# Optimization experiments

Hardware: AMD Instinct MI355X
Metric: run time of the kernel (lower is better)

Reference implementation:

```python
import jax, jax.numpy as jnp
import numpy as np

HIDDEN = 1024
HEADS = 16
HEAD_DIM = HIDDEN // HEADS

def setup_inputs() -> dict:
    key = jax.random.key(0)
    k1, k2, k3 = jax.random.split(key, 3)
    scale = 1.0 / np.sqrt(HIDDEN)
    return {
        "x": jax.random.normal(k1, (2, 2048, HIDDEN), dtype=jnp.float32),
        "w_qkv": jax.random.normal(k2, (HIDDEN, 3 * HIDDEN), dtype=jnp.float32) * scale,
        "b_qkv": jnp.zeros((3 * HIDDEN,), dtype=jnp.float32),
        "w_out": jax.random.normal(k3, (HIDDEN, HIDDEN), dtype=jnp.float32) * scale,
        "b_out": jnp.zeros((HIDDEN,), dtype=jnp.float32),
    }

def reference(x, w_qkv, b_qkv, w_out, b_out):
    B, S, H = x.shape
    qkv = x @ w_qkv + b_qkv                              # (B,S,3H)
    qkv = qkv.reshape(B, S, 3, HEADS, HEAD_DIM)
    qkv = jnp.transpose(qkv, (2, 0, 3, 1, 4))            # (3,B,nh,S,hd)
    q, k, v = qkv[0], qkv[1], qkv[2]
    scores = jnp.einsum("bhqd,bhkd->bhqk", q, k) / np.sqrt(HEAD_DIM)
    causal = jnp.triu(jnp.ones((S, S), dtype=bool), k=1)  # True above diagonal
    scores = jnp.where(causal, -jnp.inf, scores)
    attn = jax.nn.softmax(scores, axis=-1)               # dropout: eval mode (identity)
    out = jnp.einsum("bhqk,bhkd->bhqd", attn, v)
    out = jnp.transpose(out, (0, 2, 1, 3)).reshape(B, S, H)
    return out @ w_out + b_out
```

## Files before the change

### kernel.cpp

```cpp
#include <hip/hip_runtime.h>
#include <hip/hip_bf16.h>

typedef short short8 __attribute__((ext_vector_type(8)));
typedef float f32x4 __attribute__((ext_vector_type(4)));

typedef const __attribute__((address_space(1))) unsigned int* gas_ptr;
typedef __attribute__((address_space(3))) unsigned int* las_ptr;
#define ASYNC16(g, l) __builtin_amdgcn_global_load_lds((gas_ptr)(g), (las_ptr)(l), 16, 0, 0)

__device__ __forceinline__ unsigned short f2bf(float f) {
    unsigned int u = __builtin_bit_cast(unsigned int, f);
    u += 0x7fff + ((u >> 16) & 1);
    return (unsigned short)(u >> 16);
}
__device__ __forceinline__ float bf2f(unsigned short s) {
    unsigned int u = (unsigned int)s << 16;
    return __builtin_bit_cast(float, u);
}
__device__ __forceinline__ unsigned int pkbf_trunc(float lo, float hi) {
    return __builtin_amdgcn_perm(__builtin_bit_cast(unsigned int, hi),
                                 __builtin_bit_cast(unsigned int, lo), 0x07060302u);
}

__device__ __forceinline__ void transpose_tile(
    const float* __restrict__ w, unsigned short* __restrict__ wt,
    int K, int N, int k0, int n0, unsigned short* tile)
{
    for (int i = threadIdx.x; i < 64 * 64; i += 256) {
        int r = i >> 6, c = i & 63;
        tile[r * 65 + c] = f2bf(w[(size_t)(k0 + r) * N + n0 + c]);
    }
    __syncthreads();
    for (int i = threadIdx.x; i < 64 * 64; i += 256) {
        int r = i >> 6, c = i & 63;
        wt[(size_t)(n0 + r) * K + k0 + c] = tile[c * 65 + r];
    }
}

__global__ __launch_bounds__(256) void prep(
    const float* __restrict__ x, const float* __restrict__ w_qkv,
    const float* __restrict__ w_out,
    unsigned short* __restrict__ x_b, unsigned short* __restrict__ wqkv_t,
    unsigned short* __restrict__ wout_t)
{
    __shared__ unsigned short tile[64 * 65];
    int bid = blockIdx.x;
    if (bid < 4096) {
        int i = (bid * 256 + threadIdx.x) * 4;
        float4 v = *(const float4*)(x + i);
        ushort4 o;
        o.x = f2bf(v.x); o.y = f2bf(v.y); o.z = f2bf(v.z); o.w = f2bf(v.w);
        *(ushort4*)(x_b + i) = o;
    } else if (bid < 4096 + 768) {
        int t = bid - 4096;
        transpose_tile(w_qkv, wqkv_t, 1024, 3072, (t / 48) * 64, (t % 48) * 64, tile);
    } else {
        int t = bid - 4864;
        transpose_tile(w_out, wout_t, 1024, 1024, (t >> 4) * 64, (t & 15) * 64, tile);
    }
}


template<bool OUT_BF16, bool QKV>
__global__ __launch_bounds__(256, 3) void gemm_bt(
    const unsigned short* __restrict__ A,
    const unsigned short* __restrict__ Bt,
    const float* __restrict__ bias,
    void* __restrict__ C,
    unsigned short* __restrict__ vTp,
    int M, int N, int K)
{
    __shared__ __align__(16) unsigned short As[128 * 32];
    __shared__ __align__(16) unsigned short Bs[128 * 32];
    const int tid = threadIdx.x;
    const int lane = tid & 63;
    const int wave = tid >> 6;
    const int wr = wave >> 1, wc = wave & 1;
    const int m0 = blockIdx.x * 128, n0 = blockIdx.y * 128;
    const int fr = lane & 15, fq = lane >> 4;

    f32x4 acc[4][4] = {};

    const int grow = lane >> 2;
    const int gcol = (lane & 3) * 8;
    const unsigned short* Ag = A  + (size_t)(m0 + wave * 32 + grow) * K + gcol;
    const unsigned short* Bg = Bt + (size_t)(n0 + wave * 32 + grow) * K + gcol;
    unsigned short* AsW0 = As + (wave * 32) * 32;
    unsigned short* AsW1 = As + (wave * 32 + 16) * 32;
    unsigned short* BsW0 = Bs + (wave * 32) * 32;
    unsigned short* BsW1 = Bs + (wave * 32 + 16) * 32;

    for (int k0 = 0; k0 < K; k0 += 32) {
        __syncthreads();
        ASYNC16(Ag + k0,          AsW0);
        ASYNC16(Ag + 16 * K + k0, AsW1);
        ASYNC16(Bg + k0,          BsW0);
        ASYNC16(Bg + 16 * K + k0, BsW1);
        __syncthreads();

        short8 af[4], bfr[4];
#pragma unroll
        for (int i = 0; i < 4; i++)
            af[i] = *(const short8*)(As + (wr * 64 + i * 16 + fr) * 32 + fq * 8);
#pragma unroll
        for (int j = 0; j < 4; j++)
            bfr[j] = *(const short8*)(Bs + (wc * 64 + j * 16 + fr) * 32 + fq * 8);
#pragma unroll
        for (int i = 0; i < 4; i++)
#pragma unroll
            for (int j = 0; j < 4; j++)
                acc[i][j] = __builtin_amdgcn_mfma_f32_16x16x32_bf16(af[i], bfr[j], acc[i][j], 0, 0, 0);
    }

#pragma unroll
    for (int i = 0; i < 4; i++)
#pragma unroll
        for (int j = 0; j < 4; j++) {
            int col = n0 + wc * 64 + j * 16 + fr;
            float bv = bias[col];
            if (QKV && col >= 2048) {
                int hh = (col - 2048) >> 6, d = col & 63;
#pragma unroll
                for (int r = 0; r < 4; r++) {
                    int row = m0 + wr * 64 + i * 16 + fq * 4 + r;
                    int bb = row >> 11, s = row & 2047;
                    vTp[((size_t)(bb * 16 + hh) * 64 + d) * 2048 + s] = f2bf(acc[i][j][r] + bv);
                }
            } else {
                const int cstride = QKV ? 2048 : N;
#pragma unroll
                for (int r = 0; r < 4; r++) {
                    int row = m0 + wr * 64 + i * 16 + fq * 4 + r;
                    float v = acc[i][j][r] + bv;
                    if (OUT_BF16)
                        ((unsigned short*)C)[(size_t)row * cstride + col] = f2bf(v);
                    else
                        ((float*)C)[(size_t)row * cstride + col] = v;
                }
            }
        }
}


template<int RG0>
__device__ __forceinline__ void attn_step(
    const unsigned short* __restrict__ Ks0, const unsigned short* __restrict__ Ks1,
    const unsigned short* __restrict__ Vs0, const unsigned short* __restrict__ Vs1,
    unsigned short* __restrict__ Psw,
    const short8 (&qf)[4][2], const short8 ones,
    f32x4 (&o_acc)[4][4], f32x4 (&l_acc)[4],
    int j0, int fr, int fq,
    const int (&qrow0)[4], bool diagA, bool diagB)
{
    short8 kf[4][2];
#pragma unroll
    for (int t = 0; t < 4; t++) {
        kf[t][0] = *(const short8*)(Ks0 + (t * 16 + fr) * 32 + fq * 8);
        kf[t][1] = *(const short8*)(Ks1 + (t * 16 + fr) * 32 + fq * 8);
    }

#pragma unroll
    for (int rg = RG0; rg < 4; rg++) {
        f32x4 s[4];
#pragma unroll
        for (int t = 0; t < 4; t++) {
            s[t] = (f32x4){0.f, 0.f, 0.f, 0.f};
            s[t] = __builtin_amdgcn_mfma_f32_16x16x32_bf16(qf[rg][0], kf[t][0], s[t], 0, 0, 0);
            s[t] = __builtin_amdgcn_mfma_f32_16x16x32_bf16(qf[rg][1], kf[t][1], s[t], 0, 0, 0);
        }
        const bool diag = (rg < 2) ? diagA : diagB;
        unsigned short* prow = Psw + rg * (16 * 64);
        if (diag) {
#pragma unroll
            for (int t = 0; t < 4; t++) {
                float p[4];
#pragma unroll
                for (int r = 0; r < 4; r++) {
                    float v = __expf(s[t][r] * 0.125f - 8.0f);
                    if ((j0 + t * 16 + fr) > (qrow0[rg] + fq * 4 + r)) v = 0.f;
                    p[r] = v;
                }
                unsigned int pk01 = pkbf_trunc(p[0], p[1]);
                unsigned int pk23 = pkbf_trunc(p[2], p[3]);
                int base = (fq * 4) * 64 + ((t * 16 + fr + 16 * fq) & 63);
                prow[base]       = (unsigned short)pk01;
                prow[base + 64]  = (unsigned short)(pk01 >> 16);
                prow[base + 128] = (unsigned short)pk23;
                prow[base + 192] = (unsigned short)(pk23 >> 16);
            }
        } else {
#pragma unroll
            for (int t = 0; t < 4; t++) {
                float p[4];
#pragma unroll
                for (int r = 0; r < 4; r++)
                    p[r] = __expf(s[t][r] * 0.125f - 8.0f);
                unsigned int pk01 = pkbf_trunc(p[0], p[1]);
                unsigned int pk23 = pkbf_trunc(p[2], p[3]);
                int base = (fq * 4) * 64 + ((t * 16 + fr + 16 * fq) & 63);
                prow[base]       = (unsigned short)pk01;
                prow[base + 64]  = (unsigned short)(pk01 >> 16);
                prow[base + 128] = (unsigned short)pk23;
                prow[base + 192] = (unsigned short)(pk23 >> 16);
            }
        }
    }

#pragma unroll
    for (int ks = 0; ks < 2; ks++) {
        const unsigned short* Vsb = ks ? Vs1 : Vs0;
        const int colp = (ks * 32 + fq * 8 + 16 * ((fr >> 2) & 3)) & 63;
        short8 pf[4];
#pragma unroll
        for (int rg = RG0; rg < 4; rg++)
            pf[rg] = *(const short8*)(Psw + rg * (16 * 64) + fr * 64 + colp);
#pragma unroll
        for (int t = 0; t < 4; t++) {
            short8 vf = *(const short8*)(Vsb + (t * 16 + fr) * 32 + fq * 8);
#pragma unroll
            for (int rg = RG0; rg < 4; rg++)
                o_acc[rg][t] = __builtin_amdgcn_mfma_f32_16x16x32_bf16(pf[rg], vf, o_acc[rg][t], 0, 0, 0);
        }
#pragma unroll
        for (int rg = RG0; rg < 4; rg++)
            l_acc[rg] = __builtin_amdgcn_mfma_f32_16x16x32_bf16(pf[rg], ones, l_acc[rg], 0, 0, 0);
    }
}

__global__ __launch_bounds__(128, 2) void flash_attn(
    const unsigned short* __restrict__ qkv,
    const unsigned short* __restrict__ vT,
    unsigned short* __restrict__ Opart,
    float* __restrict__ lpart)
{
    const int gid = blockIdx.x;
    const int bh = gid & 31;
    const int sl = gid >> 5;
    const int p  = sl & 15;
    const int g  = sl >> 4;
    const int h = bh & 15, b = bh >> 4;
    const int tid = threadIdx.x, wave = tid >> 6, lane = tid & 63;
    const int fr = lane & 15, fq = lane >> 4;
    const size_t RS = 2048;

    const unsigned short* Qb = qkv + (size_t)b * 2048 * RS + h * 64;
    const unsigned short* Kb = Qb + 1024;
    const unsigned short* Vt = vT + (size_t)(b * 16 + h) * 64 * 2048;

    __shared__ __align__(16) unsigned short Ks[2][64 * 32];
    __shared__ __align__(16) unsigned short Vs[2][64 * 32];
    __shared__ __align__(16) unsigned short Ps[2][4 * 16 * 64];

    short8 qf[4][2];
    int qrow0[4];
#pragma unroll
    for (int rg = 0; rg < 4; rg++) {
        int qt = (rg < 2) ? p : (31 - p);
        qrow0[rg] = qt * 64 + wave * 32 + (rg & 1) * 16;
        const unsigned short* qrow = Qb + (size_t)(qrow0[rg] + fr) * RS;
        qf[rg][0] = *(const short8*)(qrow + fq * 8);
        qf[rg][1] = *(const short8*)(qrow + 32 + fq * 8);
    }
    short8 ones;
#pragma unroll
    for (int e = 0; e < 8; e++) ones[e] = (short)0x3F80;

    f32x4 o_acc[4][4] = {};
    f32x4 l_acc[4] = {};

    const int grow = lane >> 2;
    const int gcol = (lane & 3) * 8;
    const unsigned short* Kg = Kb + (size_t)(wave * 32 + grow) * RS + gcol;
    const unsigned short* Vg = Vt + (size_t)(wave * 32 + grow) * 2048 + gcol;
    unsigned short* KsW00 = Ks[0] + (wave * 32) * 32;
    unsigned short* KsW01 = Ks[0] + (wave * 32 + 16) * 32;
    unsigned short* KsW10 = Ks[1] + (wave * 32) * 32;
    unsigned short* KsW11 = Ks[1] + (wave * 32 + 16) * 32;
    unsigned short* VsW00 = Vs[0] + (wave * 32) * 32;
    unsigned short* VsW01 = Vs[0] + (wave * 32 + 16) * 32;
    unsigned short* VsW10 = Vs[1] + (wave * 32) * 32;
    unsigned short* VsW11 = Vs[1] + (wave * 32 + 16) * 32;

    const int njt = 32 - p;
    int lo = (g == 0) ? 0 : njt;
    int hi = njt;
    {
        int cum = 0;
        bool flo = (g == 0), fhi = false;
        for (int j = 0; j < njt; j++) {
            if (!flo && cum >= 44 * g)        { lo = j; flo = true; }
            if (!fhi && cum >= 44 * (g + 1))  { hi = j; fhi = true; }
            cum += (j <= p) ? 8 : 4;
        }
    }

    for (int jt = lo; jt < hi; jt++) {
        const int j0 = jt * 64;
        __syncthreads();
        ASYNC16(Kg + (size_t)j0 * RS,               KsW00);
        ASYNC16(Kg + (size_t)(j0 + 16) * RS,        KsW01);
        ASYNC16(Kg + (size_t)j0 * RS + 32,          KsW10);
        ASYNC16(Kg + (size_t)(j0 + 16) * RS + 32,   KsW11);
        ASYNC16(Vg + j0,               VsW00);
        ASYNC16(Vg + 16 * 2048 + j0,   VsW01);
        ASYNC16(Vg + j0 + 32,          VsW10);
        ASYNC16(Vg + 16 * 2048 + j0 + 32, VsW11);
        __syncthreads();

        bool diagA = (jt == p), diagB = (jt == 31 - p);
        if (jt <= p)
            attn_step<0>(Ks[0], Ks[1], Vs[0], Vs[1], Ps[wave], qf, ones,
                         o_acc, l_acc, j0, fr, fq, qrow0, diagA, diagB);
        else
            attn_step<2>(Ks[0], Ks[1], Vs[0], Vs[1], Ps[wave], qf, ones,
                         o_acc, l_acc, j0, fr, fq, qrow0, diagA, diagB);
    }

    unsigned short* Og = Opart + (size_t)g * 4096 * 1024;
    float* lg = lpart + (size_t)g * 4096 * 16;
#pragma unroll
    for (int rg = 0; rg < 4; rg++) {
#pragma unroll
        for (int t = 0; t < 4; t++)
#pragma unroll
            for (int r = 0; r < 4; r++) {
                int row = qrow0[rg] + fq * 4 + r;
                Og[(size_t)(b * 2048 + row) * 1024 + h * 64 + t * 16 + fr] = f2bf(o_acc[rg][t][r]);
            }
        if (fr == 0) {
#pragma unroll
            for (int r = 0; r < 4; r++) {
                int row = qrow0[rg] + fq * 4 + r;
                lg[(size_t)(b * 2048 + row) * 16 + h] = l_acc[rg][r];
            }
        }
    }
}

__global__ __launch_bounds__(256) void reduce_attn(
    const unsigned short* __restrict__ Opart, const float* __restrict__ lpart,
    unsigned short* __restrict__ out)
{
    const size_t OP = (size_t)4096 * 1024, LP = (size_t)4096 * 16;
    int i = (blockIdx.x * 256 + threadIdx.x) * 8;
    int row = i >> 10, h = (i & 1023) >> 6;
    float lsum = lpart[row * 16 + h] + lpart[LP + row * 16 + h] + lpart[2 * LP + row * 16 + h];
    float inv = 1.0f / lsum;
    float acc[8];
#pragma unroll
    for (int e = 0; e < 8; e++) acc[e] = 0.f;
#pragma unroll
    for (int gpart = 0; gpart < 3; gpart++) {
        ushort4 a0 = *(const ushort4*)(Opart + gpart * OP + i);
        ushort4 a1 = *(const ushort4*)(Opart + gpart * OP + i + 4);
        acc[0] += bf2f(a0.x); acc[1] += bf2f(a0.y); acc[2] += bf2f(a0.z); acc[3] += bf2f(a0.w);
        acc[4] += bf2f(a1.x); acc[5] += bf2f(a1.y); acc[6] += bf2f(a1.z); acc[7] += bf2f(a1.w);
    }
    ushort4 o0, o1;
    o0.x = f2bf(acc[0] * inv); o0.y = f2bf(acc[1] * inv);
    o0.z = f2bf(acc[2] * inv); o0.w = f2bf(acc[3] * inv);
    o1.x = f2bf(acc[4] * inv); o1.y = f2bf(acc[5] * inv);
    o1.z = f2bf(acc[6] * inv); o1.w = f2bf(acc[7] * inv);
    *(ushort4*)(out + i) = o0;
    *(ushort4*)(out + i + 4) = o1;
}

extern "C" void kernel_launch(void* const* d_in, const int* in_sizes, int n_in,
                              void* d_out, int out_size, void* d_ws, size_t ws_size,
                              hipStream_t stream) {
    const float* x      = (const float*)d_in[0];
    const float* w_qkv  = (const float*)d_in[1];
    const float* b_qkv  = (const float*)d_in[2];
    const float* w_out  = (const float*)d_in[3];
    const float* b_out  = (const float*)d_in[4];
    float* out = (float*)d_out;

    char* ws = (char*)d_ws;
    const size_t MB = 1024 * 1024;
    unsigned short* qkv    = (unsigned short*)(ws);
    unsigned short* vT     = (unsigned short*)(ws + 16 * MB);
    unsigned short* wout_t = (unsigned short*)(ws + 24 * MB);
    unsigned short* attn   = (unsigned short*)(ws + 26 * MB);
    float*          lpart  = (float*)         (ws + 34 * MB);
    unsigned short* x_b    = (unsigned short*)(ws + 36 * MB);
    unsigned short* wqkv_t = (unsigned short*)(ws + 44 * MB);
    unsigned short* Opart  = (unsigned short*)(ws + 36 * MB);

    prep<<<5120, 256, 0, stream>>>(x, w_qkv, w_out, x_b, wqkv_t, wout_t);
    gemm_bt<true, true ><<<dim3(32, 24), 256, 0, stream>>>(x_b,  wqkv_t, b_qkv, qkv, vT, 4096, 3072, 1024);
    flash_attn<<<1536, 128, 0, stream>>>(qkv, vT, Opart, lpart);
    reduce_attn<<<2048, 256, 0, stream>>>(Opart, lpart, attn);
    gemm_bt<false, false><<<dim3(32, 8),  256, 0, stream>>>(attn, wout_t, b_out, out, nullptr, 4096, 1024, 1024);
}
```

Measured before the change: 196.9 us.

## Keep attention probabilities in registers via transposed MFMA, dropping LDS staging of P

Swaps the MFMA operand order so S is computed transposed. Each lane's packed bf16 exponentials then form the B-operand fragment for the PV MFMA directly, which removes the per-wave LDS round trip for P. The LDS this frees, together with launch bounds raised to 3 blocks per SM, is meant to raise occupancy. V fragments are now assembled from two 4-element LDS reads, and the output store becomes vectorized 4-wide along head dim. This adds register pressure and more, narrower V loads, which could cause spills under the tighter launch bound.

```diff
diff --git a/kernel.cpp b/kernel.cpp
--- a/kernel.cpp
+++ b/kernel.cpp
@@ -2,6 +2,8 @@
 #include <hip/hip_bf16.h>
 
 typedef short short8 __attribute__((ext_vector_type(8)));
+typedef short short4v __attribute__((ext_vector_type(4)));
+typedef unsigned int uint4v __attribute__((ext_vector_type(4)));
 typedef float f32x4 __attribute__((ext_vector_type(4)));
 
 typedef const __attribute__((address_space(1))) unsigned int* gas_ptr;
@@ -146,7 +148,6 @@
 __device__ __forceinline__ void attn_step(
     const unsigned short* __restrict__ Ks0, const unsigned short* __restrict__ Ks1,
     const unsigned short* __restrict__ Vs0, const unsigned short* __restrict__ Vs1,
-    unsigned short* __restrict__ Psw,
     const short8 (&qf)[4][2], const short8 ones,
     f32x4 (&o_acc)[4][4], f32x4 (&l_acc)[4],
     int j0, int fr, int fq,
@@ -159,75 +160,67 @@
         kf[t][1] = *(const short8*)(Ks1 + (t * 16 + fr) * 32 + fq * 8);
     }
 
+    short8 pf[4][2];
 #pragma unroll
     for (int rg = RG0; rg < 4; rg++) {
         f32x4 s[4];
 #pragma unroll
         for (int t = 0; t < 4; t++) {
             s[t] = (f32x4){0.f, 0.f, 0.f, 0.f};
-            s[t] = __builtin_amdgcn_mfma_f32_16x16x32_bf16(qf[rg][0], kf[t][0], s[t], 0, 0, 0);
-            s[t] = __builtin_amdgcn_mfma_f32_16x16x32_bf16(qf[rg][1], kf[t][1], s[t], 0, 0, 0);
+            s[t] = __builtin_amdgcn_mfma_f32_16x16x32_bf16(kf[t][0], qf[rg][0], s[t], 0, 0, 0);
+            s[t] = __builtin_amdgcn_mfma_f32_16x16x32_bf16(kf[t][1], qf[rg][1], s[t], 0, 0, 0);
         }
         const bool diag = (rg < 2) ? diagA : diagB;
-        unsigned short* prow = Psw + rg * (16 * 64);
+        unsigned int pk[4][2];
         if (diag) {
+            const int qq = qrow0[rg] + fr;
+#pragma unroll
+            for (int t = 0; t < 4; t++) {
+                const int keyb = j0 + t * 16 + fq * 4;
+                float p[4];
+#pragma unroll
+                for (int r = 0; r < 4; r++) {
+                    float v = __expf(s[t][r] * 0.125f - 8.0f);
+                    if (keyb + r > qq) v = 0.f;
+                    p[r] = v;
+                }
+                pk[t][0] = pkbf_trunc(p[0], p[1]);
+                pk[t][1] = pkbf_trunc(p[2], p[3]);
+            }
+        } else {
 #pragma unroll
             for (int t = 0; t < 4; t++) {
                 float p[4];
 #pragma unroll
-                for (int r = 0; r < 4; r++) {
-                    float v = __expf(s[t][r] * 0.125f - 8.0f);
-                    if ((j0 + t * 16 + fr) > (qrow0[rg] + fq * 4 + r)) v = 0.f;
-                    p[r] = v;
-                }
-                unsigned int pk01 = pkbf_trunc(p[0], p[1]);
-                unsigned int pk23 = pkbf_trunc(p[2], p[3]);
-                int base = (fq * 4) * 64 + ((t * 16 + fr + 16 * fq) & 63);
-                prow[base]       = (unsigned short)pk01;
-                prow[base + 64]  = (unsigned short)(pk01 >> 16);
-                prow[base + 128] = (unsigned short)pk23;
-                prow[base + 192] = (unsigned short)(pk23 >> 16);
-            }
-        } else {
-#pragma unroll
-            for (int t = 0; t < 4; t++) {
-                float p[4];
-#pragma unroll
                 for (int r = 0; r < 4; r++)
                     p[r] = __expf(s[t][r] * 0.125f - 8.0f);
-                unsigned int pk01 = pkbf_trunc(p[0], p[1]);
-                unsigned int pk23 = pkbf_trunc(p[2], p[3]);
-                int base = (fq * 4) * 64 + ((t * 16 + fr + 16 * fq) & 63);
-                prow[base]       = (unsigned short)pk01;
-                prow[base + 64]  = (unsigned short)(pk01 >> 16);
-                prow[base + 128] = (unsigned short)pk23;
-                prow[base + 192] = (unsigned short)(pk23 >> 16);
+                pk[t][0] = pkbf_trunc(p[0], p[1]);
+                pk[t][1] = pkbf_trunc(p[2], p[3]);
             }
         }
+        pf[rg][0] = __builtin_bit_cast(short8, (uint4v){pk[0][0], pk[0][1], pk[1][0], pk[1][1]});
+        pf[rg][1] = __builtin_bit_cast(short8, (uint4v){pk[2][0], pk[2][1], pk[3][0], pk[3][1]});
     }
 
 #pragma unroll
     for (int ks = 0; ks < 2; ks++) {
         const unsigned short* Vsb = ks ? Vs1 : Vs0;
-        const int colp = (ks * 32 + fq * 8 + 16 * ((fr >> 2) & 3)) & 63;
-        short8 pf[4];
+#pragma unroll
+        for (int t = 0; t < 4; t++) {
+            short4v vlo = *(const short4v*)(Vsb + (t * 16 + fr) * 32 + fq * 4);
+            short4v vhi = *(const short4v*)(Vsb + (t * 16 + fr) * 32 + 16 + fq * 4);
+            short8 vf = (short8){vlo[0], vlo[1], vlo[2], vlo[3], vhi[0], vhi[1], vhi[2], vhi[3]};
+#pragma unroll
+            for (int rg = RG0; rg < 4; rg++)
+                o_acc[rg][t] = __builtin_amdgcn_mfma_f32_16x16x32_bf16(vf, pf[rg][ks], o_acc[rg][t], 0, 0, 0);
+        }
 #pragma unroll
         for (int rg = RG0; rg < 4; rg++)
-            pf[rg] = *(const short8*)(Psw + rg * (16 * 64) + fr * 64 + colp);
-#pragma unroll
-        for (int t = 0; t < 4; t++) {
-            short8 vf = *(const short8*)(Vsb + (t * 16 + fr) * 32 + fq * 8);
-#pragma unroll
-            for (int rg = RG0; rg < 4; rg++)
-                o_acc[rg][t] = __builtin_amdgcn_mfma_f32_16x16x32_bf16(pf[rg], vf, o_acc[rg][t], 0, 0, 0);
-        }
-#pragma unroll
-        for (int rg = RG0; rg < 4; rg++)
-            l_acc[rg] = __builtin_amdgcn_mfma_f32_16x16x32_bf16(pf[rg], ones, l_acc[rg], 0, 0, 0);
-    }
-}
-
-__global__ __launch_bounds__(128, 2) void flash_attn(
+            l_acc[rg] = __builtin_amdgcn_mfma_f32_16x16x32_bf16(ones, pf[rg][ks], l_acc[rg], 0, 0, 0);
+    }
+}
+
+__global__ __launch_bounds__(128, 3) void flash_attn(
     const unsigned short* __restrict__ qkv,
     const unsigned short* __restrict__ vT,
     unsigned short* __restrict__ Opart,
@@ -249,7 +242,6 @@
 
     __shared__ __align__(16) unsigned short Ks[2][64 * 32];
     __shared__ __align__(16) unsigned short Vs[2][64 * 32];
-    __shared__ __align__(16) unsigned short Ps[2][4 * 16 * 64];
 
     short8 qf[4][2];
     int qrow0[4];
@@ -309,10 +301,10 @@
 
         bool diagA = (jt == p), diagB = (jt == 31 - p);
         if (jt <= p)
-            attn_step<0>(Ks[0], Ks[1], Vs[0], Vs[1], Ps[wave], qf, ones,
+            attn_step<0>(Ks[0], Ks[1], Vs[0], Vs[1], qf, ones,
                          o_acc, l_acc, j0, fr, fq, qrow0, diagA, diagB);
         else
-            attn_step<2>(Ks[0], Ks[1], Vs[0], Vs[1], Ps[wave], qf, ones,
+            attn_step<2>(Ks[0], Ks[1], Vs[0], Vs[1], qf, ones,
                          o_acc, l_acc, j0, fr, fq, qrow0, diagA, diagB);
     }
 
@@ -320,20 +312,16 @@
     float* lg = lpart + (size_t)g * 4096 * 16;
 #pragma unroll
     for (int rg = 0; rg < 4; rg++) {
-#pragma unroll
-        for (int t = 0; t < 4; t++)
-#pragma unroll
-            for (int r = 0; r < 4; r++) {
-                int row = qrow0[rg] + fq * 4 + r;
-                Og[(size_t)(b * 2048 + row) * 1024 + h * 64 + t * 16 + fr] = f2bf(o_acc[rg][t][r]);
-            }
-        if (fr == 0) {
-#pragma unroll
-            for (int r = 0; r < 4; r++) {
-                int row = qrow0[rg] + fq * 4 + r;
-                lg[(size_t)(b * 2048 + row) * 16 + h] = l_acc[rg][r];
-            }
-        }
+        const size_t rowbase = (size_t)(b * 2048 + qrow0[rg] + fr) * 1024 + h * 64;
+#pragma unroll
+        for (int t = 0; t < 4; t++) {
+            ushort4 o;
+            o.x = f2bf(o_acc[rg][t][0]); o.y = f2bf(o_acc[rg][t][1]);
+            o.z = f2bf(o_acc[rg][t][2]); o.w = f2bf(o_acc[rg][t][3]);
+            *(ushort4*)(Og + rowbase + t * 16 + fq * 4) = o;
+        }
+        if (fq == 0)
+            lg[(size_t)(b * 2048 + qrow0[rg] + fr) * 16 + h] = l_acc[rg][0];
     }
 }
 
```

Result: slower. 315.1 us (+60.0%).
